# Kernel tuning notes

Hardware: AMD Instinct MI355X
Metric: run time of the kernel (lower is better)

## Reference

```python
import jax, jax.numpy as jnp
import numpy as np

S = 14          # grid size
B = 2           # boxes per cell
NCLS = 20       # number of classes
L_COORD = 5.0
L_NOOBJ = 0.5


def setup_inputs() -> dict:
    key = jax.random.key(0)
    k1, k2, k3, k4 = jax.random.split(key, 4)
    N = 4096
    pred_tensor = jax.random.uniform(k1, (N, S, S, B * 5 + NCLS), dtype=jnp.float32)
    target_boxes = jax.random.uniform(k2, (N, S, S, 4), dtype=jnp.float32)
    target_cls = jax.random.uniform(k3, (N, S, S, NCLS), dtype=jnp.float32)
    has_object_map = jax.random.randint(k4, (N, S, S), 0, 2) == 1
    return {
        "pred_tensor": pred_tensor,
        "target_boxes": target_boxes,
        "target_cls": target_cls,
        "has_object_map": has_object_map,
    }


def _yolo_loss(pred_tensor, target_boxes, target_cls, has_object_map):
    N = pred_tensor.shape[0]
    inv_n = 1.0 / N
    m = has_object_map.astype(pred_tensor.dtype)            # (N,S,S) 1 where object

    pred_boxes = pred_tensor[..., : B * 5].reshape(*pred_tensor.shape[:3], B, 5)  # (N,S,S,B,5)
    pred_cls = pred_tensor[..., B * 5:]                     # (N,S,S,20)

    # class loss over object cells (masked sum == boolean-index + sum)
    cls_loss = jnp.sum(m[..., None] * (pred_cls - target_cls) ** 2) * inv_n

    # no-object confidence loss: all B confidences at non-object cells vs 0
    conf = pred_boxes[..., 4]                               # (N,S,S,B)
    no_obj_loss = jnp.sum((1.0 - m)[..., None] * conf ** 2) * inv_n

    # per-cell IoU of each of the B predicted boxes against the target box.
    # xywh2xyxy: center x,y are divided by S; w,h used directly (as in source).
    xy = pred_boxes[..., :2] / S                            # (N,S,S,B,2)
    wh = pred_boxes[..., 2:4]                               # (N,S,S,B,2)
    p1 = xy - wh / 2
    p2 = xy + wh / 2
    t = target_boxes[..., None, :]                          # (N,S,S,1,4) treated as xyxy
    lt = jnp.maximum(p1, t[..., :2])
    rb = jnp.minimum(p2, t[..., 2:])
    iwh = jnp.clip(rb - lt, 0.0)
    inter = iwh[..., 0] * iwh[..., 1]                       # (N,S,S,B)
    area_p = wh[..., 0] * wh[..., 1]                        # (x2-x1)*(y2-y1) = w*h
    area_t = (t[..., 2] - t[..., 0]) * (t[..., 3] - t[..., 1])
    iou = inter / (area_p + area_t - inter)                 # (N,S,S,B)

    # best-of-B selection per cell (torch.max picks first max index -> argmax)
    best_idx = jnp.argmax(iou, axis=-1)                     # (N,S,S)
    best_boxes = jnp.take_along_axis(
        pred_boxes, best_idx[..., None, None], axis=3
    )[..., 0, :]                                            # (N,S,S,5)

    # containing-object confidence loss: best conf vs 1.0 at object cells
    containing_obj_loss = jnp.sum(m * (best_boxes[..., 4] - 1.0) ** 2) * inv_n

    center_loss = jnp.sum(m[..., None] * (best_boxes[..., :2] - target_boxes[..., :2]) ** 2)
    dim_loss = jnp.sum(
        m[..., None]
        * (jnp.sqrt(best_boxes[..., 2:4]) - jnp.sqrt(target_boxes[..., 2:4])) ** 2
    )
    reg_loss = (center_loss + dim_loss) * inv_n

    total_loss = cls_loss + L_NOOBJ * no_obj_loss + L_COORD * reg_loss + containing_obj_loss
    # [total, reg, containing_obj, no_obj, cls]
    return jnp.stack([total_loss, reg_loss, containing_obj_loss, no_obj_loss, cls_loss])


def reference(pred_tensor, target_boxes, target_cls, has_object_map):
    return _yolo_loss(pred_tensor, target_boxes, target_cls, has_object_map)
```

## Files before the change

kernel.cpp:

```cpp
#include <hip/hip_runtime.h>


#define NCELLS (4096 * 14 * 14)
#define NBLOCKS (NCELLS / 256)
#define NLINES 64


typedef const __attribute__((address_space(1))) void* gas_t;
typedef __attribute__((address_space(3))) void* las_t;

__device__ __forceinline__ void gload_lds16(const void* g, void* l) {
    __builtin_amdgcn_global_load_lds((gas_t)g, (las_t)l, 16, 0, 0);
}

__global__ void yolo_zero_kernel(float* __restrict__ ws) {
    const int t = threadIdx.x;
#pragma unroll
    for (int i = 0; i < 5; ++i) {
        const int k = t + 256 * i;
        if (k < 1040) ws[k] = 0.0f;
    }
}

__global__ void yolo_detect_kernel(const unsigned char* __restrict__ mb,
                                   int* __restrict__ flag) {
    int t = threadIdx.x;
    unsigned int found = 0;
#pragma unroll
    for (int k = 0; k < 16; ++k) {
        int slot = t * 16 + k;
        found |= mb[4 * slot + 1] | mb[4 * slot + 2] | mb[4 * slot + 3];
    }
    if (found) atomicOr(flag, 1);
}

__global__ __launch_bounds__(256) void yolo_main_kernel(
    const float* __restrict__ pred,
    const float* __restrict__ tbox,
    const float* __restrict__ tcls,
    const void* __restrict__ mask,
    const int* __restrict__ flag,
    float* __restrict__ ws) {
    __shared__ float sp[256 * 30 + 128];

    const int t = threadIdx.x;
    const int lane = t & 63;
    const int wid = t >> 6;
    const int c = blockIdx.x * 256 + t;

    {
        const char* gbase =
            (const char*)pred + (long long)(blockIdx.x * 256 + wid * 64) * 120;
        const char* gend = (const char*)pred + (long long)NCELLS * 120;
        char* lbase = (char*)sp + wid * 7680;
#pragma unroll
        for (int k = 0; k < 8; ++k) {
            const char* src = gbase + k * 1024 + lane * 16;
            if (src + 16 > gend) src = gend - 16;
            gload_lds16(src, lbase + k * 1024);
        }
    }

    float tc[20];
    {
        const float4* c4 = (const float4*)(tcls + (long long)20 * c);
#pragma unroll
        for (int k = 0; k < 5; ++k) {
            float4 v = c4[k];
            tc[4 * k] = v.x;
            tc[4 * k + 1] = v.y;
            tc[4 * k + 2] = v.z;
            tc[4 * k + 3] = v.w;
        }
    }
    const float4 tb = *(const float4*)(tbox + (long long)4 * c);
    const int mode = *flag;
    float m;
    if (mode) {
        m = ((const unsigned char*)mask)[c] ? 1.0f : 0.0f;
    } else {
        m = ((const int*)mask)[c] ? 1.0f : 0.0f;
    }

    asm volatile("s_waitcnt vmcnt(0)" ::: "memory");
    __builtin_amdgcn_sched_barrier(0);

    const float* pc = sp + wid * 1920 + 30 * lane;

    float s = 0.0f;
#pragma unroll
    for (int i = 0; i < 20; ++i) {
        float d = pc[10 + i] - tc[i];
        s += d * d;
    }
    float cls_s = m * s;

    float pv[10];
#pragma unroll
    for (int i = 0; i < 10; ++i) pv[i] = pc[i];

    float conf0 = pv[4], conf1 = pv[9];
    float noobj_s = (1.0f - m) * (conf0 * conf0 + conf1 * conf1);

    float iou[2];
    float at = (tb.z - tb.x) * (tb.w - tb.y);
#pragma unroll
    for (int b = 0; b < 2; ++b) {
        int base = 5 * b;
        float x = pv[base] / 14.0f;
        float y = pv[base + 1] / 14.0f;
        float w = pv[base + 2];
        float h = pv[base + 3];
        float p1x = x - w * 0.5f, p1y = y - h * 0.5f;
        float p2x = x + w * 0.5f, p2y = y + h * 0.5f;
        float ltx = fmaxf(p1x, tb.x), lty = fmaxf(p1y, tb.y);
        float rbx = fminf(p2x, tb.z), rby = fminf(p2y, tb.w);
        float iw = fmaxf(rbx - ltx, 0.0f), ih = fmaxf(rby - lty, 0.0f);
        float inter = iw * ih;
        float ap = w * h;
        iou[b] = inter / (ap + at - inter);
    }
    int best = (iou[1] > iou[0]) ? 5 : 0;
    float bx = pv[best], by = pv[best + 1], bw = pv[best + 2], bh = pv[best + 3],
          bc = pv[best + 4];

    float contain_s = m * (bc - 1.0f) * (bc - 1.0f);

    float dx = bx - tb.x, dy = by - tb.y;
    float dw = sqrtf(bw) - sqrtf(tb.z);
    float dh = sqrtf(bh) - sqrtf(tb.w);
    float reg_s = m * (dx * dx + dy * dy + dw * dw + dh * dh);

#pragma unroll
    for (int off = 32; off > 0; off >>= 1) {
        cls_s += __shfl_down(cls_s, off, 64);
        noobj_s += __shfl_down(noobj_s, off, 64);
        contain_s += __shfl_down(contain_s, off, 64);
        reg_s += __shfl_down(reg_s, off, 64);
    }
    if (lane == 0) {
        const int line = 16 * (((blockIdx.x << 2) | wid) & (NLINES - 1));
        atomicAdd(&ws[line + 0], cls_s);
        atomicAdd(&ws[line + 1], noobj_s);
        atomicAdd(&ws[line + 2], contain_s);
        atomicAdd(&ws[line + 3], reg_s);
    }
}

__global__ void yolo_final_kernel(const float* __restrict__ ws,
                                  float* __restrict__ out) {
    const int t = threadIdx.x;
    float4 v = ((const float4*)ws)[4 * t];
#pragma unroll
    for (int off = 32; off > 0; off >>= 1) {
        v.x += __shfl_down(v.x, off, 64);
        v.y += __shfl_down(v.y, off, 64);
        v.z += __shfl_down(v.z, off, 64);
        v.w += __shfl_down(v.w, off, 64);
    }
    if (t == 0) {
        const float inv_n = 1.0f / 4096.0f;
        const float cls = v.x * inv_n;
        const float noobj = v.y * inv_n;
        const float contain = v.z * inv_n;
        const float reg = v.w * inv_n;
        out[0] = cls + 0.5f * noobj + 5.0f * reg + contain;
        out[1] = reg;
        out[2] = contain;
        out[3] = noobj;
        out[4] = cls;
    }
}

extern "C" void kernel_launch(void* const* d_in, const int* in_sizes, int n_in,
                              void* d_out, int out_size, void* d_ws,
                              size_t ws_size, hipStream_t stream) {
    const float* pred = (const float*)d_in[0];
    const float* tbox = (const float*)d_in[1];
    const float* tcls = (const float*)d_in[2];
    const void* mask = d_in[3];
    float* ws = (float*)d_ws;
    float* out = (float*)d_out;

    yolo_zero_kernel<<<1, 256, 0, stream>>>(ws);
    yolo_detect_kernel<<<1, 256, 0, stream>>>((const unsigned char*)mask,
                                              (int*)(ws + 1024));
    yolo_main_kernel<<<NBLOCKS, 256, 0, stream>>>(pred, tbox, tcls, mask,
                                                  (const int*)(ws + 1024), ws);
    yolo_final_kernel<<<1, 64, 0, stream>>>(ws, out);
}
```

Before: 208.2 us.

## Double-buffer per-wave tiles so loads overlap compute across four tiles

Each wave now handles four 64-cell tiles and alternates between two LDS buffers. It issues the next tile's async global-to-LDS copy and register loads before computing the current tile, waiting only on partial vmcnt. Blocks drop to 128 threads, and there are four times fewer atomic reductions. The mask load becomes unconditional, with the index shifted by mode. This adds register pressure from the duplicated target buffers and cuts the number of resident waves, which could reduce latency hiding on a kernel that is bandwidth bound.

New measurement: 215.8 us. 3.6% more time.

```diff
diff --git a/kernel.cpp b/kernel.cpp
--- a/kernel.cpp
+++ b/kernel.cpp
@@ -2,7 +2,10 @@
 
 
 #define NCELLS (4096 * 14 * 14)
-#define NBLOCKS (NCELLS / 256)
+#define NTILES (NCELLS / 64)
+#define TPW 4
+#define NWAVES (NTILES / TPW)
+#define NBLK (NWAVES / 2)
 #define NLINES 64
 
 
@@ -34,116 +37,164 @@
     if (found) atomicOr(flag, 1);
 }
 
-__global__ __launch_bounds__(256) void yolo_main_kernel(
+
+__device__ __forceinline__ void issue_dma(const char* gpred, const char* gend,
+                                          long long cellbase, char* lb,
+                                          int lane) {
+#pragma unroll
+    for (int k = 0; k < 8; ++k) {
+        const char* src = gpred + cellbase * 120 + k * 1024 + lane * 16;
+        if (src + 16 > gend) src = gend - 16;
+        gload_lds16(src, lb + k * 1024);
+    }
+}
+
+__device__ __forceinline__ void issue_regs(const float* __restrict__ tcls,
+                                           const float* __restrict__ tbox,
+                                           const void* __restrict__ mask,
+                                           int mode, long long c,
+                                           float (&tc)[20], float4& tb,
+                                           unsigned int& b8, int& i32) {
+    const float4* c4 = (const float4*)(tcls + 20 * c);
+#pragma unroll
+    for (int k = 0; k < 5; ++k) {
+        float4 v = c4[k];
+        tc[4 * k] = v.x;
+        tc[4 * k + 1] = v.y;
+        tc[4 * k + 2] = v.z;
+        tc[4 * k + 3] = v.w;
+    }
+    tb = *(const float4*)(tbox + 4 * c);
+    b8 = ((const unsigned char*)mask)[c];
+    i32 = ((const int*)mask)[c >> (2 * mode)];
+}
+
+__device__ __forceinline__ void tile_compute(const float* __restrict__ pcb,
+                                             int lane, int mode,
+                                             const float (&tc)[20], float4 tb,
+                                             unsigned int b8, int i32,
+                                             float& a_cls, float& a_no,
+                                             float& a_cont, float& a_reg) {
+    const float m = mode ? (b8 ? 1.0f : 0.0f) : (i32 ? 1.0f : 0.0f);
+    const float* pc = pcb + 30 * lane;
+
+    float s = 0.0f;
+#pragma unroll
+    for (int i = 0; i < 20; ++i) {
+        const float d = pc[10 + i] - tc[i];
+        s += d * d;
+    }
+    a_cls += m * s;
+
+    float pv[10];
+#pragma unroll
+    for (int i = 0; i < 10; ++i) pv[i] = pc[i];
+
+    const float conf0 = pv[4], conf1 = pv[9];
+    a_no += (1.0f - m) * (conf0 * conf0 + conf1 * conf1);
+
+    float iou[2];
+    const float at = (tb.z - tb.x) * (tb.w - tb.y);
+#pragma unroll
+    for (int b = 0; b < 2; ++b) {
+        const int base = 5 * b;
+        const float x = pv[base] / 14.0f;
+        const float y = pv[base + 1] / 14.0f;
+        const float w = pv[base + 2];
+        const float h = pv[base + 3];
+        const float p1x = x - w * 0.5f, p1y = y - h * 0.5f;
+        const float p2x = x + w * 0.5f, p2y = y + h * 0.5f;
+        const float ltx = fmaxf(p1x, tb.x), lty = fmaxf(p1y, tb.y);
+        const float rbx = fminf(p2x, tb.z), rby = fminf(p2y, tb.w);
+        const float iw = fmaxf(rbx - ltx, 0.0f), ih = fmaxf(rby - lty, 0.0f);
+        const float inter = iw * ih;
+        const float ap = w * h;
+        iou[b] = inter / (ap + at - inter);
+    }
+    const int best = (iou[1] > iou[0]) ? 5 : 0;
+    const float bx = pv[best], by = pv[best + 1], bw = pv[best + 2],
+                bh = pv[best + 3], bc = pv[best + 4];
+
+    a_cont += m * (bc - 1.0f) * (bc - 1.0f);
+
+    const float dx = bx - tb.x, dy = by - tb.y;
+    const float dw = sqrtf(bw) - sqrtf(tb.z);
+    const float dh = sqrtf(bh) - sqrtf(tb.w);
+    a_reg += m * (dx * dx + dy * dy + dw * dw + dh * dh);
+}
+
+#define WAIT16()                                          \
+    asm volatile("s_waitcnt vmcnt(16)" ::: "memory");     \
+    __builtin_amdgcn_sched_barrier(0)
+#define WAIT0()                                           \
+    asm volatile("s_waitcnt vmcnt(0)" ::: "memory");      \
+    __builtin_amdgcn_sched_barrier(0)
+
+__global__ __launch_bounds__(128) void yolo_main_kernel(
     const float* __restrict__ pred,
     const float* __restrict__ tbox,
     const float* __restrict__ tcls,
     const void* __restrict__ mask,
     const int* __restrict__ flag,
     float* __restrict__ ws) {
-    __shared__ float sp[256 * 30 + 128];
+    __shared__ float sp[2][2][2048];
 
     const int t = threadIdx.x;
     const int lane = t & 63;
     const int wid = t >> 6;
-    const int c = blockIdx.x * 256 + t;
-
-    {
-        const char* gbase =
-            (const char*)pred + (long long)(blockIdx.x * 256 + wid * 64) * 120;
-        const char* gend = (const char*)pred + (long long)NCELLS * 120;
-        char* lbase = (char*)sp + wid * 7680;
-#pragma unroll
-        for (int k = 0; k < 8; ++k) {
-            const char* src = gbase + k * 1024 + lane * 16;
-            if (src + 16 > gend) src = gend - 16;
-            gload_lds16(src, lbase + k * 1024);
-        }
-    }
-
-    float tc[20];
-    {
-        const float4* c4 = (const float4*)(tcls + (long long)20 * c);
-#pragma unroll
-        for (int k = 0; k < 5; ++k) {
-            float4 v = c4[k];
-            tc[4 * k] = v.x;
-            tc[4 * k + 1] = v.y;
-            tc[4 * k + 2] = v.z;
-            tc[4 * k + 3] = v.w;
-        }
-    }
-    const float4 tb = *(const float4*)(tbox + (long long)4 * c);
+    const int wgid = blockIdx.x * 2 + wid;
+    const long long cell0 = (long long)wgid * (TPW * 64);
     const int mode = *flag;
-    float m;
-    if (mode) {
-        m = ((const unsigned char*)mask)[c] ? 1.0f : 0.0f;
-    } else {
-        m = ((const int*)mask)[c] ? 1.0f : 0.0f;
-    }
-
-    asm volatile("s_waitcnt vmcnt(0)" ::: "memory");
-    __builtin_amdgcn_sched_barrier(0);
-
-    const float* pc = sp + wid * 1920 + 30 * lane;
-
-    float s = 0.0f;
-#pragma unroll
-    for (int i = 0; i < 20; ++i) {
-        float d = pc[10 + i] - tc[i];
-        s += d * d;
-    }
-    float cls_s = m * s;
-
-    float pv[10];
-#pragma unroll
-    for (int i = 0; i < 10; ++i) pv[i] = pc[i];
-
-    float conf0 = pv[4], conf1 = pv[9];
-    float noobj_s = (1.0f - m) * (conf0 * conf0 + conf1 * conf1);
-
-    float iou[2];
-    float at = (tb.z - tb.x) * (tb.w - tb.y);
-#pragma unroll
-    for (int b = 0; b < 2; ++b) {
-        int base = 5 * b;
-        float x = pv[base] / 14.0f;
-        float y = pv[base + 1] / 14.0f;
-        float w = pv[base + 2];
-        float h = pv[base + 3];
-        float p1x = x - w * 0.5f, p1y = y - h * 0.5f;
-        float p2x = x + w * 0.5f, p2y = y + h * 0.5f;
-        float ltx = fmaxf(p1x, tb.x), lty = fmaxf(p1y, tb.y);
-        float rbx = fminf(p2x, tb.z), rby = fminf(p2y, tb.w);
-        float iw = fmaxf(rbx - ltx, 0.0f), ih = fmaxf(rby - lty, 0.0f);
-        float inter = iw * ih;
-        float ap = w * h;
-        iou[b] = inter / (ap + at - inter);
-    }
-    int best = (iou[1] > iou[0]) ? 5 : 0;
-    float bx = pv[best], by = pv[best + 1], bw = pv[best + 2], bh = pv[best + 3],
-          bc = pv[best + 4];
-
-    float contain_s = m * (bc - 1.0f) * (bc - 1.0f);
-
-    float dx = bx - tb.x, dy = by - tb.y;
-    float dw = sqrtf(bw) - sqrtf(tb.z);
-    float dh = sqrtf(bh) - sqrtf(tb.w);
-    float reg_s = m * (dx * dx + dy * dy + dw * dw + dh * dh);
+
+    const char* const gpred = (const char*)pred;
+    const char* const gend = gpred + (long long)NCELLS * 120;
+    char* const lbA = (char*)&sp[wid][0][0];
+    char* const lbB = (char*)&sp[wid][1][0];
+
+    float a_cls = 0.0f, a_no = 0.0f, a_cont = 0.0f, a_reg = 0.0f;
+    float tcA[20], tcB[20];
+    float4 tbA, tbB;
+    unsigned int b8A, b8B;
+    int i32A, i32B;
+
+    issue_dma(gpred, gend, cell0, lbA, lane);
+    issue_regs(tcls, tbox, mask, mode, cell0 + lane, tcA, tbA, b8A, i32A);
+
+    issue_dma(gpred, gend, cell0 + 64, lbB, lane);
+    issue_regs(tcls, tbox, mask, mode, cell0 + 64 + lane, tcB, tbB, b8B, i32B);
+    WAIT16();
+    tile_compute((const float*)lbA, lane, mode, tcA, tbA, b8A, i32A,
+                 a_cls, a_no, a_cont, a_reg);
+
+    issue_dma(gpred, gend, cell0 + 128, lbA, lane);
+    issue_regs(tcls, tbox, mask, mode, cell0 + 128 + lane, tcA, tbA, b8A, i32A);
+    WAIT16();
+    tile_compute((const float*)lbB, lane, mode, tcB, tbB, b8B, i32B,
+                 a_cls, a_no, a_cont, a_reg);
+
+    issue_dma(gpred, gend, cell0 + 192, lbB, lane);
+    issue_regs(tcls, tbox, mask, mode, cell0 + 192 + lane, tcB, tbB, b8B, i32B);
+    WAIT16();
+    tile_compute((const float*)lbA, lane, mode, tcA, tbA, b8A, i32A,
+                 a_cls, a_no, a_cont, a_reg);
+
+    WAIT0();
+    tile_compute((const float*)lbB, lane, mode, tcB, tbB, b8B, i32B,
+                 a_cls, a_no, a_cont, a_reg);
 
 #pragma unroll
     for (int off = 32; off > 0; off >>= 1) {
-        cls_s += __shfl_down(cls_s, off, 64);
-        noobj_s += __shfl_down(noobj_s, off, 64);
-        contain_s += __shfl_down(contain_s, off, 64);
-        reg_s += __shfl_down(reg_s, off, 64);
+        a_cls += __shfl_down(a_cls, off, 64);
+        a_no += __shfl_down(a_no, off, 64);
+        a_cont += __shfl_down(a_cont, off, 64);
+        a_reg += __shfl_down(a_reg, off, 64);
     }
     if (lane == 0) {
-        const int line = 16 * (((blockIdx.x << 2) | wid) & (NLINES - 1));
-        atomicAdd(&ws[line + 0], cls_s);
-        atomicAdd(&ws[line + 1], noobj_s);
-        atomicAdd(&ws[line + 2], contain_s);
-        atomicAdd(&ws[line + 3], reg_s);
+        const int line = 16 * (wgid & (NLINES - 1));
+        atomicAdd(&ws[line + 0], a_cls);
+        atomicAdd(&ws[line + 1], a_no);
+        atomicAdd(&ws[line + 2], a_cont);
+        atomicAdd(&ws[line + 3], a_reg);
     }
 }
 
@@ -185,7 +236,7 @@
     yolo_zero_kernel<<<1, 256, 0, stream>>>(ws);
     yolo_detect_kernel<<<1, 256, 0, stream>>>((const unsigned char*)mask,
                                               (int*)(ws + 1024));
-    yolo_main_kernel<<<NBLOCKS, 256, 0, stream>>>(pred, tbox, tcls, mask,
-                                                  (const int*)(ws + 1024), ws);
+    yolo_main_kernel<<<NBLK, 128, 0, stream>>>(pred, tbox, tcls, mask,
+                                               (const int*)(ws + 1024), ws);
     yolo_final_kernel<<<1, 64, 0, stream>>>(ws, out);
 }
```
